# Kernel optimization log

Hardware: AMD Instinct MI355X
Metric: run time of the kernel (lower is better)

The kernel has to match this reference:

```python
import jax, jax.numpy as jnp
import numpy as np

V, ENC, D, E = 10000, 2048, 512, 512
B, L = 128, 64


def setup_inputs() -> dict:
    key = jax.random.key(0)
    ks = jax.random.split(key, 12)
    s = lambda *sh: 1.0 / np.sqrt(sh[-1])
    return {
        "global_feats": jax.random.normal(ks[0], (B, ENC), jnp.float32),
        "encoded_captions": jax.random.randint(ks[1], (B, L), 0, V, jnp.int64),
        "caption_lengths": jax.random.randint(ks[2], (B,), 1, L, jnp.int64),
        "W_embed": jax.random.normal(ks[3], (V, E), jnp.float32) * 0.02,
        "W_init": jax.random.normal(ks[4], (D, ENC), jnp.float32) * s(ENC),
        "b_init": jnp.zeros((D,), jnp.float32),
        "W_ih": jax.random.normal(ks[5], (3 * D, E), jnp.float32) * s(E),
        "W_hh": jax.random.normal(ks[6], (3 * D, D), jnp.float32) * s(D),
        "b_ih": jnp.zeros((3 * D,), jnp.float32),
        "b_hh": jnp.zeros((3 * D,), jnp.float32),
        "W_fc": jax.random.normal(ks[7], (V, D), jnp.float32) * s(D),
        "b_fc": jnp.zeros((V,), jnp.float32),
    }


def reference(global_feats, encoded_captions, caption_lengths,
              W_embed, W_init, b_init, W_ih, W_hh, b_ih, b_hh, W_fc, b_fc):
    # init_hidden: h0 = tanh(Linear(global_feats))  -> (B, D)
    h0 = jnp.tanh(global_feats @ W_init.T + b_init)

    # teacher forcing over timesteps 0..L-2 (PyTorch GRU gate order: r, z, n)
    emb = W_embed[encoded_captions[:, : L - 1]]          # (B, L-1, E)
    gi = jnp.einsum('ble,ge->blg', emb, W_ih) + b_ih     # (B, L-1, 3D) precomputed input gates
    gi = jnp.swapaxes(gi, 0, 1)                          # (L-1, B, 3D) scan over time

    def step(h, gi_t):
        gh = h @ W_hh.T + b_hh                           # (B, 3D)
        i_r, i_z, i_n = jnp.split(gi_t, 3, axis=-1)
        h_r, h_z, h_n = jnp.split(gh, 3, axis=-1)
        r = jax.nn.sigmoid(i_r + h_r)
        z = jax.nn.sigmoid(i_z + h_z)
        n = jnp.tanh(i_n + r * h_n)
        h_new = (1.0 - z) * n + z * h
        return h_new, h_new

    _, hs = jax.lax.scan(step, h0, gi)                   # hs: (L-1, B, D)
    # dropout is identity in eval/reference mode
    logits = jnp.einsum('lbd,vd->blv', hs, W_fc) + b_fc  # (B, L-1, V)
    return logits, caption_lengths - 1
```

## Files before the change

kernel.cpp:

```cpp
#include <hip/hip_runtime.h>
#include <hip/hip_bf16.h>

#define V_    10000
#define ENC_  2048
#define D_    512
#define B_    128
#define L_    64
#define T_    63
#define M_    (B_ * L_ - B_)
#define G_    (3 * D_)
#define LOGITS_SZ ((long)M_ * V_)
#define SCAN_NB 64

typedef __bf16 bf16x8_t __attribute__((ext_vector_type(8)));
typedef float  f32x4_t  __attribute__((ext_vector_type(4)));
typedef short  s16x8_t  __attribute__((ext_vector_type(8)));
typedef unsigned long long ull_t;

typedef __attribute__((address_space(3))) char*       lds_cptr_t;
typedef const __attribute__((address_space(1))) char* glb_cptr_t;

__device__ __forceinline__ void gload_lds16(const void* g, void* l) {
  __builtin_amdgcn_global_load_lds((glb_cptr_t)g, (lds_cptr_t)l, 16, 0, 0);
}
__device__ __forceinline__ float bf2f(short s) {
  return __uint_as_float(((unsigned)(unsigned short)s) << 16);
}
__device__ __forceinline__ short f2bf(float f) {
  __hip_bfloat16 h = __float2bfloat16(f);
  return *reinterpret_cast<short*>(&h);
}
__device__ __forceinline__ s16x8_t cvt8(const float* p) {
  f32x4_t lo = *reinterpret_cast<const f32x4_t*>(p);
  f32x4_t hi = *reinterpret_cast<const f32x4_t*>(p + 4);
  s16x8_t r;
#pragma unroll
  for (int e = 0; e < 4; e++) { r[e] = f2bf(lo[e]); r[4 + e] = f2bf(hi[e]); }
  return r;
}
__device__ __forceinline__ float sigmoidf_(float x) {
  return 1.0f / (1.0f + __expf(-x));
}
__device__ __forceinline__ bf16x8_t lds_frag(const short* p) {
  return __builtin_bit_cast(bf16x8_t, *reinterpret_cast<const s16x8_t*>(p));
}

__global__ void GG_cvt5(const float* __restrict__ whh, __hip_bfloat16* __restrict__ dwhh,
                        const float* __restrict__ wih, __hip_bfloat16* __restrict__ dwih,
                        const float* __restrict__ wemb, __hip_bfloat16* __restrict__ dwemb,
                        const float* __restrict__ winit, __hip_bfloat16* __restrict__ dwinit,
                        const float* __restrict__ gf, __hip_bfloat16* __restrict__ dgf) {
  const int i = blockIdx.x * blockDim.x + threadIdx.x;
  const float* s; __hip_bfloat16* d; int off;
  if (i < 98304)        { s = whh;   d = dwhh;   off = i; }
  else if (i < 196608)  { s = wih;   d = dwih;   off = i - 98304; }
  else if (i < 836608)  { s = wemb;  d = dwemb;  off = i - 196608; }
  else if (i < 967680)  { s = winit; d = dwinit; off = i - 836608; }
  else                  { s = gf;    d = dgf;    off = i - 967680; }
  s16x8_t v = cvt8(s + (long)off * 8);
  *reinterpret_cast<s16x8_t*>(d + (long)off * 8) = v;
}

__global__ void GG_cvt_kernel(const float* __restrict__ src,
                              __hip_bfloat16* __restrict__ dst, int n8) {
  int i = blockIdx.x * blockDim.x + threadIdx.x;
  if (i < n8) {
    s16x8_t v = cvt8(src + (long)i * 8);
    *reinterpret_cast<s16x8_t*>(dst + (long)i * 8) = v;
  }
}

__global__ __launch_bounds__(256) void GG_gemm_h0(
    const __hip_bfloat16* __restrict__ gfB,
    const __hip_bfloat16* __restrict__ WinitB,
    const float* __restrict__ binit,
    __hip_bfloat16* __restrict__ hfull) {
  __shared__ short sA[128 * 64];
  __shared__ short sB[128 * 64];
  const int lane = threadIdx.x & 63;
  const int wave = threadIdx.x >> 6;
  const int n0 = blockIdx.x * 128;
  const int srow = lane >> 3;
  const int scol = (lane & 7) * 8;

  f32x4_t acc[4][4] = {};

  const __hip_bfloat16* aptr[4];
  const __hip_bfloat16* bptr[4];
#pragma unroll
  for (int i = 0; i < 4; i++) {
    const int r = (wave * 4 + i) * 8 + srow;
    aptr[i] = gfB + (long)r * ENC_ + scol;
    bptr[i] = WinitB + (long)(n0 + r) * ENC_ + scol;
  }

  const int wm = (wave >> 1) * 64;
  const int wn = (wave & 1) * 64;
  const int fr = lane & 15;
  const int fk = (lane >> 4) * 8;

  for (int kt = 0; kt < 32; kt++) {
    __syncthreads();
#pragma unroll
    for (int i = 0; i < 4; i++) {
      const int chunk = wave * 4 + i;
      gload_lds16(aptr[i] + kt * 64, sA + chunk * 512);
      gload_lds16(bptr[i] + kt * 64, sB + chunk * 512);
    }
    __syncthreads();
#pragma unroll
    for (int kk = 0; kk < 2; kk++) {
      bf16x8_t a[4], b[4];
#pragma unroll
      for (int i = 0; i < 4; i++) {
        a[i] = lds_frag(sA + (wm + i * 16 + fr) * 64 + kk * 32 + fk);
        b[i] = lds_frag(sB + (wn + i * 16 + fr) * 64 + kk * 32 + fk);
      }
#pragma unroll
      for (int i = 0; i < 4; i++)
#pragma unroll
        for (int j = 0; j < 4; j++)
          acc[i][j] = __builtin_amdgcn_mfma_f32_16x16x32_bf16(a[i], b[j], acc[i][j], 0, 0, 0);
    }
  }

  const int fq = lane >> 4;
#pragma unroll
  for (int j = 0; j < 4; j++) {
    const int n = n0 + wn + j * 16 + fr;
    const float bv = binit[n];
#pragma unroll
    for (int i = 0; i < 4; i++)
#pragma unroll
      for (int rr = 0; rr < 4; rr++) {
        const int m = wm + i * 16 + fq * 4 + rr;
        hfull[(long)m * 64 * 512 + n] = __float2bfloat16(tanhf(acc[i][j][rr] + bv));
      }
  }
}

__global__ __launch_bounds__(256) void GG_gemm_gi(
    const __hip_bfloat16* __restrict__ WembB,
    const int* __restrict__ cap,
    const __hip_bfloat16* __restrict__ WihB,
    const float* __restrict__ bias,
    __hip_bfloat16* __restrict__ C) {
  __shared__ short sA[128 * 64];
  __shared__ short sB[128 * 64];
  const int lane = threadIdx.x & 63;
  const int wave = threadIdx.x >> 6;
  const int m0 = blockIdx.y * 128;
  const int n0 = blockIdx.x * 128;
  const int srow = lane >> 3;
  const int scol = (lane & 7) * 8;

  f32x4_t acc[4][4] = {};

  const __hip_bfloat16* aptr[4];
  const __hip_bfloat16* bptr[4];
#pragma unroll
  for (int i = 0; i < 4; i++) {
    const int r = (wave * 4 + i) * 8 + srow;
    const int bt = m0 + r;
    const int bb = bt / 63;
    const int tt = bt - bb * 63;
    aptr[i] = WembB + (long)cap[bb * L_ + tt] * 512 + scol;
    bptr[i] = WihB + (long)(n0 + r) * 512 + scol;
  }

  const int wm = (wave >> 1) * 64;
  const int wn = (wave & 1) * 64;
  const int fr = lane & 15;
  const int fk = (lane >> 4) * 8;

  for (int kt = 0; kt < 8; kt++) {
    __syncthreads();
#pragma unroll
    for (int i = 0; i < 4; i++) {
      const int chunk = wave * 4 + i;
      gload_lds16(aptr[i] + kt * 64, sA + chunk * 512);
      gload_lds16(bptr[i] + kt * 64, sB + chunk * 512);
    }
    __syncthreads();
#pragma unroll
    for (int kk = 0; kk < 2; kk++) {
      bf16x8_t a[4], b[4];
#pragma unroll
      for (int i = 0; i < 4; i++) {
        a[i] = lds_frag(sA + (wm + i * 16 + fr) * 64 + kk * 32 + fk);
        b[i] = lds_frag(sB + (wn + i * 16 + fr) * 64 + kk * 32 + fk);
      }
#pragma unroll
      for (int i = 0; i < 4; i++)
#pragma unroll
        for (int j = 0; j < 4; j++)
          acc[i][j] = __builtin_amdgcn_mfma_f32_16x16x32_bf16(a[i], b[j], acc[i][j], 0, 0, 0);
    }
  }

  const int fq = lane >> 4;
#pragma unroll
  for (int j = 0; j < 4; j++) {
    const int n = n0 + wn + j * 16 + fr;
    const float bv = bias[n];
#pragma unroll
    for (int i = 0; i < 4; i++)
#pragma unroll
      for (int rr = 0; rr < 4; rr++) {
        const int m = m0 + wm + i * 16 + fq * 4 + rr;
        C[(long)m * G_ + n] = __float2bfloat16(acc[i][j][rr] + bv);
      }
  }
}

template <bool BBF16>
__global__ __launch_bounds__(256) void GG_gemm_logits(
    const __hip_bfloat16* __restrict__ hfull,
    const void* __restrict__ Bsrc,
    const float* __restrict__ bias,
    float* __restrict__ C) {
  const int flat = blockIdx.x;
  const int xcd = flat & 7;
  const int s = flat >> 3;
  const int col = xcd * 10 + s % 10;
  const int row = s / 10;
  if (col >= 79) return;
  const int m0 = row * 128;
  const int n0 = col * 128;

  __shared__ short sA[128 * 64];
  __shared__ short sB[128 * 64];
  const int lane = threadIdx.x & 63;
  const int wave = threadIdx.x >> 6;
  const int srow = lane >> 3;
  const int scol = (lane & 7) * 8;

  f32x4_t acc[4][4] = {};

  const __hip_bfloat16* aptr[4];
  const __hip_bfloat16* bptrB[4];
  const float* bptrF[4];
#pragma unroll
  for (int i = 0; i < 4; i++) {
    const int r = (wave * 4 + i) * 8 + srow;
    const int m = m0 + r;
    const int bb = m / 63;
    const int tt = m - bb * 63;
    aptr[i] = hfull + ((long)bb * 64 + tt + 1) * 512 + scol;
    int nrow = n0 + r;
    nrow = (nrow < V_) ? nrow : (V_ - 1);
    if constexpr (BBF16) bptrB[i] = (const __hip_bfloat16*)Bsrc + (long)nrow * 512 + scol;
    else                 bptrF[i] = (const float*)Bsrc + (long)nrow * 512 + scol;
  }

  const int wm = (wave >> 1) * 64;
  const int wn = (wave & 1) * 64;
  const int fr = lane & 15;
  const int fk = (lane >> 4) * 8;

  for (int kt = 0; kt < 8; kt++) {
    s16x8_t vb[4];
    if constexpr (!BBF16) {
#pragma unroll
      for (int i = 0; i < 4; i++) vb[i] = cvt8(bptrF[i] + kt * 64);
    }
    __syncthreads();
#pragma unroll
    for (int i = 0; i < 4; i++) {
      const int chunk = wave * 4 + i;
      gload_lds16(aptr[i] + kt * 64, sA + chunk * 512);
      if constexpr (BBF16)
        gload_lds16(bptrB[i] + kt * 64, sB + chunk * 512);
      else
        *reinterpret_cast<s16x8_t*>(sB + chunk * 512 + lane * 8) = vb[i];
    }
    __syncthreads();
#pragma unroll
    for (int kk = 0; kk < 2; kk++) {
      bf16x8_t a[4], b[4];
#pragma unroll
      for (int i = 0; i < 4; i++) {
        a[i] = lds_frag(sA + (wm + i * 16 + fr) * 64 + kk * 32 + fk);
        b[i] = lds_frag(sB + (wn + i * 16 + fr) * 64 + kk * 32 + fk);
      }
#pragma unroll
      for (int i = 0; i < 4; i++)
#pragma unroll
        for (int j = 0; j < 4; j++)
          acc[i][j] = __builtin_amdgcn_mfma_f32_16x16x32_bf16(a[i], b[j], acc[i][j], 0, 0, 0);
    }
  }

  const int fq = lane >> 4;
#pragma unroll
  for (int j = 0; j < 4; j++) {
    const int n = n0 + wn + j * 16 + fr;
    if (n >= V_) continue;
    const float bv = bias[n];
#pragma unroll
    for (int i = 0; i < 4; i++)
#pragma unroll
      for (int rr = 0; rr < 4; rr++) {
        const int m = m0 + wm + i * 16 + fq * 4 + rr;
        C[(long)m * V_ + n] = acc[i][j][rr] + bv;
      }
  }
}

__global__ __launch_bounds__(256) void GG_scan_persist(
    __hip_bfloat16* __restrict__ hfull,
    const __hip_bfloat16* __restrict__ gi,
    const __hip_bfloat16* __restrict__ WhhB,
    const float* __restrict__ bhh,
    int* __restrict__ flagbase) {
  __shared__ short sW[48 * 512];
  const int lane = threadIdx.x & 63;
  const int wave = threadIdx.x >> 6;
  const int strip = blockIdx.x & 31;
  const int half  = blockIdx.x >> 5;
  const int d0 = strip * 16;
  const int fr = lane & 15;
  const int g4 = lane >> 4;
  int* myflags = flagbase + half * 32;

  for (int rr = wave; rr < 48; rr += 4) {
    const int grow = (rr >> 4) * 512 + d0 + (rr & 15);
    gload_lds16(WhhB + (long)grow * 512 + (lane ^ (rr & 7)) * 8, sW + rr * 512);
  }

  const int dd = d0 + fr;
  const int bbase = half * 64 + wave * 16 + g4 * 4;
  const float br_ = bhh[dd], bz_ = bhh[512 + dd], bn_ = bhh[1024 + dd];
  const short* gis = (const short*)gi;

  const int arow = half * 64 + wave * 16 + fr;
  const ull_t abase0 =
      (ull_t)hfull + ((ull_t)arow * 64 * 512 + (unsigned)(g4 * 8)) * 2ull;

  ull_t sbase[4];
  const short* gp0[4];
#pragma unroll
  for (int rr = 0; rr < 4; rr++) {
    sbase[rr] = (ull_t)hfull +
                ((ull_t)(bbase + rr) * 64 * 512 + (unsigned)dd) * 2ull;
    gp0[rr] = gis + (long)(bbase + rr) * T_ * G_ + dd;
  }

  unsigned cr[4], cz[4], cn[4];
  float hp[4];
#pragma unroll
  for (int rr = 0; rr < 4; rr++) {
    cr[rr] = (unsigned short)gp0[rr][0];
    cz[rr] = (unsigned short)gp0[rr][512];
    cn[rr] = (unsigned short)gp0[rr][1024];
    hp[rr] = bf2f(*(const short*)&hfull[((long)(bbase + rr) * 64) * 512 + dd]);
  }

  asm volatile("s_waitcnt vmcnt(0)" ::: "memory");
  __syncthreads();

  for (int t = 0; t < T_; t++) {
    if (t > 0) {
      while (true) {
        const int v = __hip_atomic_load(&myflags[lane & 31], __ATOMIC_RELAXED,
                                        __HIP_MEMORY_SCOPE_SYSTEM);
        if (__all(v >= t)) break;
        __builtin_amdgcn_s_sleep(1);
      }
    }

    const ull_t ab = abase0 + (ull_t)t * 1024ull;
    f32x4_t a[16];
#define ALOAD(IDX, OFF)                                                        \
    asm volatile("global_load_dwordx4 %0, %1, off offset:" #OFF " sc0 sc1"     \
                 : "=v"(a[IDX]) : "v"(ab));
    ALOAD(0, 0)    ALOAD(1, 64)   ALOAD(2, 128)  ALOAD(3, 192)
    ALOAD(4, 256)  ALOAD(5, 320)  ALOAD(6, 384)  ALOAD(7, 448)
    ALOAD(8, 512)  ALOAD(9, 576)  ALOAD(10, 640) ALOAD(11, 704)
    ALOAD(12, 768) ALOAD(13, 832) ALOAD(14, 896) ALOAD(15, 960)
#undef ALOAD

    const int tp = (t < T_ - 1) ? (t + 1) : (T_ - 1);
    unsigned nr[4], nz[4], nn[4];
#pragma unroll
    for (int rr = 0; rr < 4; rr++) {
      const short* gp = gp0[rr] + (long)tp * G_;
      asm volatile("global_load_ushort %0, %1, off"             : "=v"(nr[rr]) : "v"(gp));
      asm volatile("global_load_ushort %0, %1, off offset:1024" : "=v"(nz[rr]) : "v"(gp));
      asm volatile("global_load_ushort %0, %1, off offset:2048" : "=v"(nn[rr]) : "v"(gp));
    }

    asm volatile("s_waitcnt vmcnt(12)" ::: "memory");
    __builtin_amdgcn_sched_barrier(0);

    f32x4_t acc[3] = {};
#pragma unroll
    for (int kt = 0; kt < 16; kt++) {
      const bf16x8_t afr = __builtin_bit_cast(bf16x8_t, a[kt]);
      const int gsw = ((kt * 4 + g4) ^ (fr & 7)) * 8;
      bf16x8_t bfr[3];
#pragma unroll
      for (int j = 0; j < 3; j++) bfr[j] = lds_frag(sW + (j * 16 + fr) * 512 + gsw);
#pragma unroll
      for (int j = 0; j < 3; j++)
        acc[j] = __builtin_amdgcn_mfma_f32_16x16x32_bf16(afr, bfr[j], acc[j], 0, 0, 0);
    }

#pragma unroll
    for (int rr = 0; rr < 4; rr++) {
      const float rg = sigmoidf_(bf2f((short)cr[rr]) + acc[0][rr] + br_);
      const float zg = sigmoidf_(bf2f((short)cz[rr]) + acc[1][rr] + bz_);
      const float ng = tanhf(bf2f((short)cn[rr]) + rg * (acc[2][rr] + bn_));
      const short hnb = f2bf((1.f - zg) * ng + zg * hp[rr]);
      hp[rr] = bf2f(hnb);
      const ull_t saddr = sbase[rr] + (ull_t)(t + 1) * 1024ull;
      const unsigned int val = (unsigned short)hnb;
      asm volatile("global_store_short %0, %1, off sc0 sc1"
                   :: "v"(saddr), "v"(val) : "memory");
    }

    asm volatile("s_waitcnt vmcnt(0)" ::: "memory");
    __builtin_amdgcn_sched_barrier(0);
#pragma unroll
    for (int rr = 0; rr < 4; rr++) { cr[rr] = nr[rr]; cz[rr] = nz[rr]; cn[rr] = nn[rr]; }

    if (t < T_ - 1) {
      __syncthreads();
      if (threadIdx.x == 0)
        __hip_atomic_store(&myflags[strip], t + 1, __ATOMIC_RELAXED,
                           __HIP_MEMORY_SCOPE_SYSTEM);
    }
  }
}

__global__ void GG_tail_kernel(const int* __restrict__ lens, float* __restrict__ out) {
  const int b = threadIdx.x;
  if (b < B_) out[LOGITS_SZ + b] = (float)(lens[b] - 1);
}

extern "C" void kernel_launch(void* const* d_in, const int* in_sizes, int n_in,
                              void* d_out, int out_size, void* d_ws, size_t ws_size,
                              hipStream_t stream) {
  const float* gf      = (const float*)d_in[0];
  const int*   cap     = (const int*)d_in[1];
  const int*   lens    = (const int*)d_in[2];
  const float* W_embed = (const float*)d_in[3];
  const float* W_init  = (const float*)d_in[4];
  const float* b_init  = (const float*)d_in[5];
  const float* W_ih    = (const float*)d_in[6];
  const float* W_hh    = (const float*)d_in[7];
  const float* b_ih    = (const float*)d_in[8];
  const float* b_hh    = (const float*)d_in[9];
  const float* W_fc    = (const float*)d_in[10];
  const float* b_fc    = (const float*)d_in[11];
  float* out = (float*)d_out;

  char* ob = (char*)d_out;
  __hip_bfloat16* gi_ws  = (__hip_bfloat16*)ob;
  __hip_bfloat16* WhhB   = (__hip_bfloat16*)(ob + 25165824);
  __hip_bfloat16* WihB   = (__hip_bfloat16*)(ob + 27262976);
  __hip_bfloat16* WembB  = (__hip_bfloat16*)(ob + 29360128);
  __hip_bfloat16* WinitB = (__hip_bfloat16*)(ob + 40894464);
  __hip_bfloat16* gfB    = (__hip_bfloat16*)(ob + 43253760);

  __hip_bfloat16* hfull = (__hip_bfloat16*)d_ws;
  __hip_bfloat16* WfcB  = (__hip_bfloat16*)((char*)d_ws + 8388608);
  const bool big_ws = ws_size >= (size_t)(8388608 + 10240000 + 256);
  int* flags = (int*)((char*)d_ws + (big_ws ? 18628608 : 8388608));

  hipMemsetAsync(flags, 0, 256, stream);

  GG_cvt5<<<dim3(3908), 256, 0, stream>>>(W_hh, WhhB, W_ih, WihB, W_embed, WembB,
                                          W_init, WinitB, gf, gfB);
  if (big_ws)
    GG_cvt_kernel<<<dim3((V_ * D_ / 8 + 255) / 256), 256, 0, stream>>>(W_fc, WfcB, V_ * D_ / 8);

  GG_gemm_h0<<<dim3(4), 256, 0, stream>>>(gfB, WinitB, b_init, hfull);

  GG_gemm_gi<<<dim3(G_ / 128, M_ / 128), 256, 0, stream>>>(WembB, cap, WihB, b_ih, gi_ws);

  GG_scan_persist<<<dim3(SCAN_NB), 256, 0, stream>>>(hfull, gi_ws, WhhB, b_hh, flags);

  if (big_ws)
    GG_gemm_logits<true><<<dim3(5040), 256, 0, stream>>>(hfull, WfcB, b_fc, out);
  else
    GG_gemm_logits<false><<<dim3(5040), 256, 0, stream>>>(hfull, W_fc, b_fc, out);

  GG_tail_kernel<<<dim3(1), 128, 0, stream>>>(lens, out);
}
```

Before: 558.3 us.

## Overlap logits GEMM with GRU scan via flag-synchronized worker blocks

Merges the persistent GRU scan and the output-projection GEMM into one launch. Extra worker blocks poll the per-timestep flags and compute each timestep's logits as soon as its hidden state is written, so the vocabulary GEMM runs during the latency-bound scan instead of after it. This needs a larger workspace for gi and the converted W_fc, and falls back to the old separate path when the workspace is too small. Risks include worker blocks competing with scan blocks for CUs, polling traffic, and a smaller per-step GEMM tile with less reuse.

```diff
diff --git a/kernel.cpp b/kernel.cpp
--- a/kernel.cpp
+++ b/kernel.cpp
@@ -10,7 +10,8 @@
 #define M_    (B_ * L_ - B_)
 #define G_    (3 * D_)
 #define LOGITS_SZ ((long)M_ * V_)
-#define SCAN_NB 64
+#define NSCAN 64
+#define NWORK 158
 
 typedef __bf16 bf16x8_t __attribute__((ext_vector_type(8)));
 typedef float  f32x4_t  __attribute__((ext_vector_type(4)));
@@ -307,128 +308,222 @@
   }
 }
 
-__global__ __launch_bounds__(256) void GG_scan_persist(
+__global__ __launch_bounds__(256) void GG_scan_logits(
     __hip_bfloat16* __restrict__ hfull,
     const __hip_bfloat16* __restrict__ gi,
     const __hip_bfloat16* __restrict__ WhhB,
     const float* __restrict__ bhh,
-    int* __restrict__ flagbase) {
-  __shared__ short sW[48 * 512];
+    int* __restrict__ flagbase,
+    const __hip_bfloat16* __restrict__ WfcB,
+    const float* __restrict__ bfc,
+    float* __restrict__ C) {
+  __shared__ short smem[48 * 512];
   const int lane = threadIdx.x & 63;
   const int wave = threadIdx.x >> 6;
-  const int strip = blockIdx.x & 31;
-  const int half  = blockIdx.x >> 5;
-  const int d0 = strip * 16;
   const int fr = lane & 15;
   const int g4 = lane >> 4;
-  int* myflags = flagbase + half * 32;
-
-  for (int rr = wave; rr < 48; rr += 4) {
-    const int grow = (rr >> 4) * 512 + d0 + (rr & 15);
-    gload_lds16(WhhB + (long)grow * 512 + (lane ^ (rr & 7)) * 8, sW + rr * 512);
-  }
-
-  const int dd = d0 + fr;
-  const int bbase = half * 64 + wave * 16 + g4 * 4;
-  const float br_ = bhh[dd], bz_ = bhh[512 + dd], bn_ = bhh[1024 + dd];
-  const short* gis = (const short*)gi;
-
-  const int arow = half * 64 + wave * 16 + fr;
-  const ull_t abase0 =
-      (ull_t)hfull + ((ull_t)arow * 64 * 512 + (unsigned)(g4 * 8)) * 2ull;
-
-  ull_t sbase[4];
-  const short* gp0[4];
-#pragma unroll
-  for (int rr = 0; rr < 4; rr++) {
-    sbase[rr] = (ull_t)hfull +
-                ((ull_t)(bbase + rr) * 64 * 512 + (unsigned)dd) * 2ull;
-    gp0[rr] = gis + (long)(bbase + rr) * T_ * G_ + dd;
-  }
-
-  unsigned cr[4], cz[4], cn[4];
-  float hp[4];
-#pragma unroll
-  for (int rr = 0; rr < 4; rr++) {
-    cr[rr] = (unsigned short)gp0[rr][0];
-    cz[rr] = (unsigned short)gp0[rr][512];
-    cn[rr] = (unsigned short)gp0[rr][1024];
-    hp[rr] = bf2f(*(const short*)&hfull[((long)(bbase + rr) * 64) * 512 + dd]);
-  }
-
-  asm volatile("s_waitcnt vmcnt(0)" ::: "memory");
-  __syncthreads();
-
-  for (int t = 0; t < T_; t++) {
-    if (t > 0) {
-      while (true) {
-        const int v = __hip_atomic_load(&myflags[lane & 31], __ATOMIC_RELAXED,
-                                        __HIP_MEMORY_SCOPE_SYSTEM);
-        if (__all(v >= t)) break;
-        __builtin_amdgcn_s_sleep(1);
-      }
-    }
-
-    const ull_t ab = abase0 + (ull_t)t * 1024ull;
-    f32x4_t a[16];
+
+  if (blockIdx.x < NSCAN) {
+    short* sW = smem;
+    const int strip = blockIdx.x & 31;
+    const int half  = blockIdx.x >> 5;
+    const int d0 = strip * 16;
+    int* myflags = flagbase + half * 32;
+
+    for (int rr = wave; rr < 48; rr += 4) {
+      const int grow = (rr >> 4) * 512 + d0 + (rr & 15);
+      gload_lds16(WhhB + (long)grow * 512 + (lane ^ (rr & 7)) * 8, sW + rr * 512);
+    }
+
+    const int dd = d0 + fr;
+    const int bbase = half * 64 + wave * 16 + g4 * 4;
+    const float br_ = bhh[dd], bz_ = bhh[512 + dd], bn_ = bhh[1024 + dd];
+    const short* gis = (const short*)gi;
+
+    const int arow = half * 64 + wave * 16 + fr;
+    const ull_t abase0 =
+        (ull_t)hfull + ((ull_t)arow * 64 * 512 + (unsigned)(g4 * 8)) * 2ull;
+
+    ull_t sbase[4];
+    const short* gp0[4];
+#pragma unroll
+    for (int rr = 0; rr < 4; rr++) {
+      sbase[rr] = (ull_t)hfull +
+                  ((ull_t)(bbase + rr) * 64 * 512 + (unsigned)dd) * 2ull;
+      gp0[rr] = gis + (long)(bbase + rr) * T_ * G_ + dd;
+    }
+
+    unsigned cr[4], cz[4], cn[4];
+    float hp[4];
+#pragma unroll
+    for (int rr = 0; rr < 4; rr++) {
+      cr[rr] = (unsigned short)gp0[rr][0];
+      cz[rr] = (unsigned short)gp0[rr][512];
+      cn[rr] = (unsigned short)gp0[rr][1024];
+      hp[rr] = bf2f(*(const short*)&hfull[((long)(bbase + rr) * 64) * 512 + dd]);
+    }
+
+    asm volatile("s_waitcnt vmcnt(0)" ::: "memory");
+    __syncthreads();
+
+    for (int t = 0; t < T_; t++) {
+      if (t > 0) {
+        while (true) {
+          const int v = __hip_atomic_load(&myflags[lane & 31], __ATOMIC_RELAXED,
+                                          __HIP_MEMORY_SCOPE_SYSTEM);
+          if (__all(v >= t)) break;
+          __builtin_amdgcn_s_sleep(1);
+        }
+      }
+
+      const ull_t ab = abase0 + (ull_t)t * 1024ull;
+      f32x4_t a[16];
 #define ALOAD(IDX, OFF)                                                        \
-    asm volatile("global_load_dwordx4 %0, %1, off offset:" #OFF " sc0 sc1"     \
-                 : "=v"(a[IDX]) : "v"(ab));
-    ALOAD(0, 0)    ALOAD(1, 64)   ALOAD(2, 128)  ALOAD(3, 192)
-    ALOAD(4, 256)  ALOAD(5, 320)  ALOAD(6, 384)  ALOAD(7, 448)
-    ALOAD(8, 512)  ALOAD(9, 576)  ALOAD(10, 640) ALOAD(11, 704)
-    ALOAD(12, 768) ALOAD(13, 832) ALOAD(14, 896) ALOAD(15, 960)
+      asm volatile("global_load_dwordx4 %0, %1, off offset:" #OFF " sc0 sc1"   \
+                   : "=v"(a[IDX]) : "v"(ab));
+      ALOAD(0, 0)    ALOAD(1, 64)   ALOAD(2, 128)  ALOAD(3, 192)
+      ALOAD(4, 256)  ALOAD(5, 320)  ALOAD(6, 384)  ALOAD(7, 448)
+      ALOAD(8, 512)  ALOAD(9, 576)  ALOAD(10, 640) ALOAD(11, 704)
+      ALOAD(12, 768) ALOAD(13, 832) ALOAD(14, 896) ALOAD(15, 960)
 #undef ALOAD
 
-    const int tp = (t < T_ - 1) ? (t + 1) : (T_ - 1);
-    unsigned nr[4], nz[4], nn[4];
-#pragma unroll
-    for (int rr = 0; rr < 4; rr++) {
-      const short* gp = gp0[rr] + (long)tp * G_;
-      asm volatile("global_load_ushort %0, %1, off"             : "=v"(nr[rr]) : "v"(gp));
-      asm volatile("global_load_ushort %0, %1, off offset:1024" : "=v"(nz[rr]) : "v"(gp));
-      asm volatile("global_load_ushort %0, %1, off offset:2048" : "=v"(nn[rr]) : "v"(gp));
-    }
-
-    asm volatile("s_waitcnt vmcnt(12)" ::: "memory");
-    __builtin_amdgcn_sched_barrier(0);
-
-    f32x4_t acc[3] = {};
-#pragma unroll
-    for (int kt = 0; kt < 16; kt++) {
-      const bf16x8_t afr = __builtin_bit_cast(bf16x8_t, a[kt]);
-      const int gsw = ((kt * 4 + g4) ^ (fr & 7)) * 8;
-      bf16x8_t bfr[3];
-#pragma unroll
-      for (int j = 0; j < 3; j++) bfr[j] = lds_frag(sW + (j * 16 + fr) * 512 + gsw);
-#pragma unroll
-      for (int j = 0; j < 3; j++)
-        acc[j] = __builtin_amdgcn_mfma_f32_16x16x32_bf16(afr, bfr[j], acc[j], 0, 0, 0);
-    }
-
-#pragma unroll
-    for (int rr = 0; rr < 4; rr++) {
-      const float rg = sigmoidf_(bf2f((short)cr[rr]) + acc[0][rr] + br_);
-      const float zg = sigmoidf_(bf2f((short)cz[rr]) + acc[1][rr] + bz_);
-      const float ng = tanhf(bf2f((short)cn[rr]) + rg * (acc[2][rr] + bn_));
-      const short hnb = f2bf((1.f - zg) * ng + zg * hp[rr]);
-      hp[rr] = bf2f(hnb);
-      const ull_t saddr = sbase[rr] + (ull_t)(t + 1) * 1024ull;
-      const unsigned int val = (unsigned short)hnb;
-      asm volatile("global_store_short %0, %1, off sc0 sc1"
-                   :: "v"(saddr), "v"(val) : "memory");
-    }
-
-    asm volatile("s_waitcnt vmcnt(0)" ::: "memory");
-    __builtin_amdgcn_sched_barrier(0);
-#pragma unroll
-    for (int rr = 0; rr < 4; rr++) { cr[rr] = nr[rr]; cz[rr] = nz[rr]; cn[rr] = nn[rr]; }
-
-    if (t < T_ - 1) {
+      const int tp = (t < T_ - 1) ? (t + 1) : (T_ - 1);
+      unsigned nr[4], nz[4], nn[4];
+#pragma unroll
+      for (int rr = 0; rr < 4; rr++) {
+        const short* gp = gp0[rr] + (long)tp * G_;
+        asm volatile("global_load_ushort %0, %1, off"             : "=v"(nr[rr]) : "v"(gp));
+        asm volatile("global_load_ushort %0, %1, off offset:1024" : "=v"(nz[rr]) : "v"(gp));
+        asm volatile("global_load_ushort %0, %1, off offset:2048" : "=v"(nn[rr]) : "v"(gp));
+      }
+
+      asm volatile("s_waitcnt vmcnt(12)" ::: "memory");
+      __builtin_amdgcn_sched_barrier(0);
+
+      f32x4_t acc[3] = {};
+#pragma unroll
+      for (int kt = 0; kt < 16; kt++) {
+        const bf16x8_t afr = __builtin_bit_cast(bf16x8_t, a[kt]);
+        const int gsw = ((kt * 4 + g4) ^ (fr & 7)) * 8;
+        bf16x8_t bfr[3];
+#pragma unroll
+        for (int j = 0; j < 3; j++) bfr[j] = lds_frag(sW + (j * 16 + fr) * 512 + gsw);
+#pragma unroll
+        for (int j = 0; j < 3; j++)
+          acc[j] = __builtin_amdgcn_mfma_f32_16x16x32_bf16(afr, bfr[j], acc[j], 0, 0, 0);
+      }
+
+#pragma unroll
+      for (int rr = 0; rr < 4; rr++) {
+        const float rg = sigmoidf_(bf2f((short)cr[rr]) + acc[0][rr] + br_);
+        const float zg = sigmoidf_(bf2f((short)cz[rr]) + acc[1][rr] + bz_);
+        const float ng = tanhf(bf2f((short)cn[rr]) + rg * (acc[2][rr] + bn_));
+        const short hnb = f2bf((1.f - zg) * ng + zg * hp[rr]);
+        hp[rr] = bf2f(hnb);
+        const ull_t saddr = sbase[rr] + (ull_t)(t + 1) * 1024ull;
+        const unsigned int val = (unsigned short)hnb;
+        asm volatile("global_store_short %0, %1, off sc0 sc1"
+                     :: "v"(saddr), "v"(val) : "memory");
+      }
+
+      asm volatile("s_waitcnt vmcnt(0)" ::: "memory");
+      __builtin_amdgcn_sched_barrier(0);
+#pragma unroll
+      for (int rr = 0; rr < 4; rr++) { cr[rr] = nr[rr]; cz[rr] = nz[rr]; cn[rr] = nn[rr]; }
+
       __syncthreads();
       if (threadIdx.x == 0)
         __hip_atomic_store(&myflags[strip], t + 1, __ATOMIC_RELAXED,
                            __HIP_MEMORY_SCOPE_SYSTEM);
+    }
+  } else {
+    const int w = blockIdx.x - NSCAN;
+    const int hh = w & 1;
+    const int nb = w >> 1;
+    const int n0 = nb * 128;
+    short* sA = smem;
+    short* sB = smem + 64 * 64;
+    int* myflags = flagbase + hh * 32;
+
+    const int srow = lane >> 3;
+    const int scol = (lane & 7) * 8;
+    const int wm = (wave >> 1) * 32;
+    const int wn = (wave & 1) * 64;
+    const int fk = g4 * 8;
+    const int fq = g4;
+
+    const __hip_bfloat16* bptr[4];
+#pragma unroll
+    for (int i = 0; i < 4; i++) {
+      int nrow = n0 + (wave * 4 + i) * 8 + srow;
+      nrow = (nrow < V_) ? nrow : (V_ - 1);
+      bptr[i] = WfcB + (long)nrow * 512 + scol;
+    }
+    const __hip_bfloat16* abase[2];
+#pragma unroll
+    for (int i = 0; i < 2; i++) {
+      const int b = hh * 64 + (wave * 2 + i) * 8 + srow;
+      abase[i] = hfull + (long)b * 64 * 512 + scol;
+    }
+    float bv[4];
+#pragma unroll
+    for (int j = 0; j < 4; j++) {
+      const int n = n0 + wn + j * 16 + fr;
+      bv[j] = bfc[(n < V_) ? n : (V_ - 1)];
+    }
+
+    for (int t = 0; t < T_; t++) {
+      while (true) {
+        const int v = __hip_atomic_load(&myflags[lane & 31], __ATOMIC_RELAXED,
+                                        __HIP_MEMORY_SCOPE_SYSTEM);
+        if (__all(v >= t + 1)) break;
+        __builtin_amdgcn_s_sleep(32);
+      }
+
+      f32x4_t acc[2][4] = {};
+      for (int kt = 0; kt < 8; kt++) {
+        __syncthreads();
+#pragma unroll
+        for (int i = 0; i < 2; i++) {
+          const int chunk = wave * 2 + i;
+          gload_lds16(abase[i] + (long)(t + 1) * 512 + kt * 64, sA + chunk * 512);
+        }
+#pragma unroll
+        for (int i = 0; i < 4; i++) {
+          const int chunk = wave * 4 + i;
+          gload_lds16(bptr[i] + kt * 64, sB + chunk * 512);
+        }
+        __syncthreads();
+#pragma unroll
+        for (int kk = 0; kk < 2; kk++) {
+          bf16x8_t a[2], b[4];
+#pragma unroll
+          for (int i = 0; i < 2; i++)
+            a[i] = lds_frag(sA + (wm + i * 16 + fr) * 64 + kk * 32 + fk);
+#pragma unroll
+          for (int j = 0; j < 4; j++)
+            b[j] = lds_frag(sB + (wn + j * 16 + fr) * 64 + kk * 32 + fk);
+#pragma unroll
+          for (int i = 0; i < 2; i++)
+#pragma unroll
+            for (int j = 0; j < 4; j++)
+              acc[i][j] = __builtin_amdgcn_mfma_f32_16x16x32_bf16(a[i], b[j], acc[i][j], 0, 0, 0);
+        }
+      }
+      __syncthreads();
+
+#pragma unroll
+      for (int j = 0; j < 4; j++) {
+        const int n = n0 + wn + j * 16 + fr;
+        if (n >= V_) continue;
+#pragma unroll
+        for (int i = 0; i < 2; i++)
+#pragma unroll
+          for (int rr = 0; rr < 4; rr++) {
+            const int b = hh * 64 + wm + i * 16 + fq * 4 + rr;
+            C[((long)b * 63 + t) * V_ + n] = acc[i][j][rr] + bv[j];
+          }
+      }
     }
   }
 }
@@ -456,35 +551,50 @@
   float* out = (float*)d_out;
 
   char* ob = (char*)d_out;
-  __hip_bfloat16* gi_ws  = (__hip_bfloat16*)ob;
   __hip_bfloat16* WhhB   = (__hip_bfloat16*)(ob + 25165824);
   __hip_bfloat16* WihB   = (__hip_bfloat16*)(ob + 27262976);
   __hip_bfloat16* WembB  = (__hip_bfloat16*)(ob + 29360128);
   __hip_bfloat16* WinitB = (__hip_bfloat16*)(ob + 40894464);
   __hip_bfloat16* gfB    = (__hip_bfloat16*)(ob + 43253760);
 
-  __hip_bfloat16* hfull = (__hip_bfloat16*)d_ws;
-  __hip_bfloat16* WfcB  = (__hip_bfloat16*)((char*)d_ws + 8388608);
-  const bool big_ws = ws_size >= (size_t)(8388608 + 10240000 + 256);
-  int* flags = (int*)((char*)d_ws + (big_ws ? 18628608 : 8388608));
+  char* ws = (char*)d_ws;
+  __hip_bfloat16* hfull = (__hip_bfloat16*)ws;
+  const bool overlap = ws_size >= (size_t)43401728;
+  const bool bigws   = ws_size >= (size_t)18628864;
+  int* flags;
+  __hip_bfloat16* WfcB = nullptr;
+  __hip_bfloat16* giP;
+  if (overlap) {
+    flags = (int*)(ws + 8388608);
+    WfcB  = (__hip_bfloat16*)(ws + 8389120);
+    giP   = (__hip_bfloat16*)(ws + 18629120);
+  } else {
+    giP = (__hip_bfloat16*)d_out;
+    if (bigws) { WfcB = (__hip_bfloat16*)(ws + 8388608); flags = (int*)(ws + 18628608); }
+    else       { flags = (int*)(ws + 8388608); }
+  }
 
   hipMemsetAsync(flags, 0, 256, stream);
 
   GG_cvt5<<<dim3(3908), 256, 0, stream>>>(W_hh, WhhB, W_ih, WihB, W_embed, WembB,
                                           W_init, WinitB, gf, gfB);
-  if (big_ws)
+  if (overlap || bigws)
     GG_cvt_kernel<<<dim3((V_ * D_ / 8 + 255) / 256), 256, 0, stream>>>(W_fc, WfcB, V_ * D_ / 8);
 
   GG_gemm_h0<<<dim3(4), 256, 0, stream>>>(gfB, WinitB, b_init, hfull);
 
-  GG_gemm_gi<<<dim3(G_ / 128, M_ / 128), 256, 0, stream>>>(WembB, cap, WihB, b_ih, gi_ws);
-
-  GG_scan_persist<<<dim3(SCAN_NB), 256, 0, stream>>>(hfull, gi_ws, WhhB, b_hh, flags);
-
-  if (big_ws)
-    GG_gemm_logits<true><<<dim3(5040), 256, 0, stream>>>(hfull, WfcB, b_fc, out);
-  else
-    GG_gemm_logits<false><<<dim3(5040), 256, 0, stream>>>(hfull, W_fc, b_fc, out);
+  GG_gemm_gi<<<dim3(G_ / 128, M_ / 128), 256, 0, stream>>>(WembB, cap, WihB, b_ih, giP);
+
+  const int nblk = overlap ? (NSCAN + NWORK) : NSCAN;
+  GG_scan_logits<<<dim3(nblk), 256, 0, stream>>>(hfull, giP, WhhB, b_hh, flags,
+                                                 WfcB, b_fc, out);
+
+  if (!overlap) {
+    if (bigws)
+      GG_gemm_logits<true><<<dim3(5040), 256, 0, stream>>>(hfull, WfcB, b_fc, out);
+    else
+      GG_gemm_logits<false><<<dim3(5040), 256, 0, stream>>>(hfull, W_fc, b_fc, out);
+  }
 
   GG_tail_kernel<<<dim3(1), 128, 0, stream>>>(lens, out);
 }
```

Result: slower. 627.4 us (+12.4%).

## Replace scan flag barriers with sentinel-polled hidden state in time-major layout

Applied to the files above, without the earlier changes.

The persistent GRU scan no longer uses per-strip atomic flags and block barriers to signal step completion. The hidden-state buffer is pre-filled with 0xFF (a NaN bf16 sentinel), and each wave spins re-loading its h(t) slice until no element carries the sentinel bits. The hidden buffer also moves from batch-major to time-major so each step's rows are contiguous, and the h0 and logits GEMM indexing is updated to match. This removes the store-wait, __syncthreads and flag round trip from the critical path, but adds a memset and relies on bf16 outputs never matching the sentinel bit pattern.

```diff
diff --git a/kernel.cpp b/kernel.cpp
--- a/kernel.cpp
+++ b/kernel.cpp
@@ -15,6 +15,7 @@
 typedef __bf16 bf16x8_t __attribute__((ext_vector_type(8)));
 typedef float  f32x4_t  __attribute__((ext_vector_type(4)));
 typedef short  s16x8_t  __attribute__((ext_vector_type(8)));
+typedef unsigned u32x4_t __attribute__((ext_vector_type(4)));
 typedef unsigned long long ull_t;
 
 typedef __attribute__((address_space(3))) char*       lds_cptr_t;
@@ -134,7 +135,7 @@
 #pragma unroll
       for (int rr = 0; rr < 4; rr++) {
         const int m = wm + i * 16 + fq * 4 + rr;
-        hfull[(long)m * 64 * 512 + n] = __float2bfloat16(tanhf(acc[i][j][rr] + bv));
+        hfull[(long)m * 512 + n] = __float2bfloat16(tanhf(acc[i][j][rr] + bv));
       }
   }
 }
@@ -246,7 +247,7 @@
     const int m = m0 + r;
     const int bb = m / 63;
     const int tt = m - bb * 63;
-    aptr[i] = hfull + ((long)bb * 64 + tt + 1) * 512 + scol;
+    aptr[i] = hfull + ((long)(tt + 1) * 128 + bb) * 512 + scol;
     int nrow = n0 + r;
     nrow = (nrow < V_) ? nrow : (V_ - 1);
     if constexpr (BBF16) bptrB[i] = (const __hip_bfloat16*)Bsrc + (long)nrow * 512 + scol;
@@ -311,8 +312,7 @@
     __hip_bfloat16* __restrict__ hfull,
     const __hip_bfloat16* __restrict__ gi,
     const __hip_bfloat16* __restrict__ WhhB,
-    const float* __restrict__ bhh,
-    int* __restrict__ flagbase) {
+    const float* __restrict__ bhh) {
   __shared__ short sW[48 * 512];
   const int lane = threadIdx.x & 63;
   const int wave = threadIdx.x >> 6;
@@ -321,7 +321,6 @@
   const int d0 = strip * 16;
   const int fr = lane & 15;
   const int g4 = lane >> 4;
-  int* myflags = flagbase + half * 32;
 
   for (int rr = wave; rr < 48; rr += 4) {
     const int grow = (rr >> 4) * 512 + d0 + (rr & 15);
@@ -335,14 +334,13 @@
 
   const int arow = half * 64 + wave * 16 + fr;
   const ull_t abase0 =
-      (ull_t)hfull + ((ull_t)arow * 64 * 512 + (unsigned)(g4 * 8)) * 2ull;
+      (ull_t)hfull + ((ull_t)arow * 512 + (unsigned)(g4 * 8)) * 2ull;
 
   ull_t sbase[4];
   const short* gp0[4];
 #pragma unroll
   for (int rr = 0; rr < 4; rr++) {
-    sbase[rr] = (ull_t)hfull +
-                ((ull_t)(bbase + rr) * 64 * 512 + (unsigned)dd) * 2ull;
+    sbase[rr] = (ull_t)hfull + ((ull_t)(bbase + rr) * 512 + (unsigned)dd) * 2ull;
     gp0[rr] = gis + (long)(bbase + rr) * T_ * G_ + dd;
   }
 
@@ -353,33 +351,13 @@
     cr[rr] = (unsigned short)gp0[rr][0];
     cz[rr] = (unsigned short)gp0[rr][512];
     cn[rr] = (unsigned short)gp0[rr][1024];
-    hp[rr] = bf2f(*(const short*)&hfull[((long)(bbase + rr) * 64) * 512 + dd]);
+    hp[rr] = bf2f(*(const short*)&hfull[(long)(bbase + rr) * 512 + dd]);
   }
 
   asm volatile("s_waitcnt vmcnt(0)" ::: "memory");
   __syncthreads();
 
   for (int t = 0; t < T_; t++) {
-    if (t > 0) {
-      while (true) {
-        const int v = __hip_atomic_load(&myflags[lane & 31], __ATOMIC_RELAXED,
-                                        __HIP_MEMORY_SCOPE_SYSTEM);
-        if (__all(v >= t)) break;
-        __builtin_amdgcn_s_sleep(1);
-      }
-    }
-
-    const ull_t ab = abase0 + (ull_t)t * 1024ull;
-    f32x4_t a[16];
-#define ALOAD(IDX, OFF)                                                        \
-    asm volatile("global_load_dwordx4 %0, %1, off offset:" #OFF " sc0 sc1"     \
-                 : "=v"(a[IDX]) : "v"(ab));
-    ALOAD(0, 0)    ALOAD(1, 64)   ALOAD(2, 128)  ALOAD(3, 192)
-    ALOAD(4, 256)  ALOAD(5, 320)  ALOAD(6, 384)  ALOAD(7, 448)
-    ALOAD(8, 512)  ALOAD(9, 576)  ALOAD(10, 640) ALOAD(11, 704)
-    ALOAD(12, 768) ALOAD(13, 832) ALOAD(14, 896) ALOAD(15, 960)
-#undef ALOAD
-
     const int tp = (t < T_ - 1) ? (t + 1) : (T_ - 1);
     unsigned nr[4], nz[4], nn[4];
 #pragma unroll
@@ -390,7 +368,27 @@
       asm volatile("global_load_ushort %0, %1, off offset:2048" : "=v"(nn[rr]) : "v"(gp));
     }
 
-    asm volatile("s_waitcnt vmcnt(12)" ::: "memory");
+    const ull_t ab = abase0 + (ull_t)t * 131072ull;
+    f32x4_t a[16];
+    while (true) {
+#define ALOAD(IDX, OFF)                                                        \
+      asm volatile("global_load_dwordx4 %0, %1, off offset:" #OFF " sc0 sc1"   \
+                   : "=v"(a[IDX]) : "v"(ab));
+      ALOAD(0, 0)    ALOAD(1, 64)   ALOAD(2, 128)  ALOAD(3, 192)
+      ALOAD(4, 256)  ALOAD(5, 320)  ALOAD(6, 384)  ALOAD(7, 448)
+      ALOAD(8, 512)  ALOAD(9, 576)  ALOAD(10, 640) ALOAD(11, 704)
+      ALOAD(12, 768) ALOAD(13, 832) ALOAD(14, 896) ALOAD(15, 960)
+#undef ALOAD
+      asm volatile("s_waitcnt vmcnt(0)" ::: "memory");
+      unsigned acc_or = 0;
+#pragma unroll
+      for (int kt = 0; kt < 16; kt++) {
+        const u32x4_t u = __builtin_bit_cast(u32x4_t, a[kt]);
+        acc_or |= u[0] | u[1] | u[2] | u[3];
+      }
+      if (__all((acc_or & 0x40004000u) == 0u)) break;
+      __builtin_amdgcn_s_sleep(2);
+    }
     __builtin_amdgcn_sched_barrier(0);
 
     f32x4_t acc[3] = {};
@@ -413,23 +411,14 @@
       const float ng = tanhf(bf2f((short)cn[rr]) + rg * (acc[2][rr] + bn_));
       const short hnb = f2bf((1.f - zg) * ng + zg * hp[rr]);
       hp[rr] = bf2f(hnb);
-      const ull_t saddr = sbase[rr] + (ull_t)(t + 1) * 1024ull;
+      const ull_t saddr = sbase[rr] + (ull_t)(t + 1) * 131072ull;
       const unsigned int val = (unsigned short)hnb;
       asm volatile("global_store_short %0, %1, off sc0 sc1"
                    :: "v"(saddr), "v"(val) : "memory");
     }
 
-    asm volatile("s_waitcnt vmcnt(0)" ::: "memory");
-    __builtin_amdgcn_sched_barrier(0);
 #pragma unroll
     for (int rr = 0; rr < 4; rr++) { cr[rr] = nr[rr]; cz[rr] = nz[rr]; cn[rr] = nn[rr]; }
-
-    if (t < T_ - 1) {
-      __syncthreads();
-      if (threadIdx.x == 0)
-        __hip_atomic_store(&myflags[strip], t + 1, __ATOMIC_RELAXED,
-                           __HIP_MEMORY_SCOPE_SYSTEM);
-    }
   }
 }
 
@@ -465,10 +454,9 @@
 
   __hip_bfloat16* hfull = (__hip_bfloat16*)d_ws;
   __hip_bfloat16* WfcB  = (__hip_bfloat16*)((char*)d_ws + 8388608);
-  const bool big_ws = ws_size >= (size_t)(8388608 + 10240000 + 256);
-  int* flags = (int*)((char*)d_ws + (big_ws ? 18628608 : 8388608));
-
-  hipMemsetAsync(flags, 0, 256, stream);
+  const bool big_ws = ws_size >= (size_t)(8388608 + 10240000);
+
+  hipMemsetAsync((char*)hfull + 131072, 0xFF, 8257536, stream);
 
   GG_cvt5<<<dim3(3908), 256, 0, stream>>>(W_hh, WhhB, W_ih, WihB, W_embed, WembB,
                                           W_init, WinitB, gf, gfB);
@@ -479,7 +467,7 @@
 
   GG_gemm_gi<<<dim3(G_ / 128, M_ / 128), 256, 0, stream>>>(WembB, cap, WihB, b_ih, gi_ws);
 
-  GG_scan_persist<<<dim3(SCAN_NB), 256, 0, stream>>>(hfull, gi_ws, WhhB, b_hh, flags);
+  GG_scan_persist<<<dim3(SCAN_NB), 256, 0, stream>>>(hfull, gi_ws, WhhB, b_hh);
 
   if (big_ws)
     GG_gemm_logits<true><<<dim3(5040), 256, 0, stream>>>(hfull, WfcB, b_fc, out);
```

Measured after the change: 597.4 us. 1.07x slower.
